# Optimization experiments

Hardware: AMD Instinct MI355X
Metric: run time of the kernel (lower is better)

## Reference

```python
import jax, jax.numpy as jnp
import numpy as np

N = 200000   # nodes
E = 6400000  # edges
F = 128      # input features
H = 16       # hidden dim (fixed in module)
C = 10       # num classes
B = 512      # graphs in batch


def setup_inputs() -> dict:
    key = jax.random.key(0)
    ks = jax.random.split(key, 9)
    x = jax.random.normal(ks[0], (N, F), dtype=jnp.float32)
    edge_index = jax.random.randint(ks[1], (2, E), 0, N, dtype=jnp.int64)
    batch = jnp.sort(jax.random.randint(ks[2], (N,), 0, B, dtype=jnp.int64))
    W1 = jax.random.normal(ks[3], (F, H), dtype=jnp.float32) * 0.1
    b1 = jnp.zeros((H,), dtype=jnp.float32)
    W2 = jax.random.normal(ks[4], (H, H), dtype=jnp.float32) * 0.1
    b2 = jnp.zeros((H,), dtype=jnp.float32)
    Wfc = jax.random.normal(ks[5], (H, C), dtype=jnp.float32) * 0.1
    bfc = jnp.zeros((C,), dtype=jnp.float32)
    return {"x": x, "edge_index": edge_index, "batch": batch,
            "W1": W1, "b1": b1, "W2": W2, "b2": b2, "Wfc": Wfc, "bfc": bfc}


def reference(x, edge_index, batch, W1, b1, W2, b2, Wfc, bfc):
    row, col = edge_index[0], edge_index[1]  # source -> target
    ones_e = jnp.ones((E,), dtype=x.dtype)
    # GCN symmetric norm with implicit self-loops: deg = 1 + in-degree
    deg = 1.0 + jax.ops.segment_sum(ones_e, col, num_segments=N)
    dis = deg ** -0.5                         # [N]
    norm = dis[row] * dis[col]                # [E], self-loop norm = 1/deg

    def gcn_conv(h, W, b):
        hw = h @ W                             # [N, out]
        msg = norm[:, None] * hw[row]          # [E, out]
        agg = jax.ops.segment_sum(msg, col, num_segments=N)
        agg = agg + hw * (1.0 / deg)[:, None]  # self-loop contribution
        return agg + b

    h = jax.nn.relu(gcn_conv(x, W1, b1))
    h = gcn_conv(h, W2, b2)
    # global mean pool over graphs
    ones_n = jnp.ones((N,), dtype=h.dtype)
    counts = jax.ops.segment_sum(ones_n, batch, num_segments=B)
    sums = jax.ops.segment_sum(h, batch, num_segments=B)
    pooled = sums / jnp.maximum(counts, 1.0)[:, None]  # [B, H]
    return pooled @ Wfc + bfc                           # [B, C]
```

## Files before the change

kernel.cpp:

```cpp
#include <hip/hip_runtime.h>

#define N_ 200000
#define E_ 6400000
#define F_ 128
#define H_ 16
#define C_ 10
#define B_ 512

#define CSH   15
#define NCH   7
#define SBSH  11
#define NSB   98
#define NKEY  (NCH * NSB)
#define NT    256
#define EPT   25000
#define N1    (N_ + 1)
#define AGGB  1563
#define G1B   1563
#define QSTR  516

__global__ __launch_bounds__(1024) void k_count1(const int* __restrict__ row, const int* __restrict__ col,
                                                 int* __restrict__ cnt1) {
    __shared__ int hist[NKEY];
    int tid = threadIdx.x, tile = blockIdx.x;
    for (int i = tid; i < NKEY; i += 1024) hist[i] = 0;
    __syncthreads();
    const int* r = row + (size_t)tile * EPT;
    const int* c = col + (size_t)tile * EPT;
    for (int i = tid; i < EPT; i += 1024) {
        int key = (r[i] >> CSH) * NSB + (c[i] >> SBSH);
        atomicAdd(&hist[key], 1);
    }
    __syncthreads();
    for (int i = tid; i < NKEY; i += 1024) cnt1[(size_t)i * NT + tile] = hist[i];
}

__global__ __launch_bounds__(256) void k_scan_col(int* __restrict__ cnt_mat, int* __restrict__ keyTotal) {
    __shared__ int s[256];
    int k = blockIdx.x, t = threadIdx.x;
    int v[4];
    int seg = 0;
#pragma unroll
    for (int j = 0; j < 4; ++j) {
        int idx = 4 * t + j;
        v[j] = (idx < NT) ? cnt_mat[(size_t)k * NT + idx] : 0;
        seg += v[j];
    }
    s[t] = seg;
    __syncthreads();
    for (int off = 1; off < 256; off <<= 1) {
        int tmp = (t >= off) ? s[t - off] : 0;
        __syncthreads();
        s[t] += tmp;
        __syncthreads();
    }
    if (t == 255) keyTotal[k] = s[255];
    int running = s[t] - seg;
#pragma unroll
    for (int j = 0; j < 4; ++j) {
        int idx = 4 * t + j;
        if (idx < NT) {
            int old = v[j];
            cnt_mat[(size_t)k * NT + idx] = running;
            running += old;
        }
    }
}

__global__ __launch_bounds__(1024) void k_scan_top(const int* __restrict__ keyTotal, int* __restrict__ keyStart, int n) {
    __shared__ int s[1024];
    int t = threadIdx.x;
    int v = (t < n) ? keyTotal[t] : 0;
    s[t] = v;
    __syncthreads();
    for (int off = 1; off < 1024; off <<= 1) {
        int tmp = (t >= off) ? s[t - off] : 0;
        __syncthreads();
        s[t] += tmp;
        __syncthreads();
    }
    if (t < n) keyStart[t] = s[t] - v;
    if (t == n - 1) keyStart[n] = s[t];
}

__global__ __launch_bounds__(1024) void k_part1(const int* __restrict__ row, const int* __restrict__ col,
                                                const int* __restrict__ cnt1, const int* __restrict__ ks1,
                                                unsigned int* __restrict__ esrc) {
    __shared__ int cur[NKEY];
    int tid = threadIdx.x, tile = blockIdx.x;
    for (int i = tid; i < NKEY; i += 1024) cur[i] = cnt1[(size_t)i * NT + tile] + ks1[i];
    __syncthreads();
    const int* r = row + (size_t)tile * EPT;
    const int* c = col + (size_t)tile * EPT;
    for (int i = tid; i < EPT; i += 1024) {
        int src = r[i], dst = c[i];
        int key = (src >> CSH) * NSB + (dst >> SBSH);
        int p = atomicAdd(&cur[key], 1);
        esrc[p] = ((unsigned int)(dst & 2047) << CSH) | (unsigned int)(src & 32767);
    }
}

__global__ __launch_bounds__(512) void k_part2(const unsigned int* __restrict__ esrc, const int* __restrict__ ks1,
                                               unsigned short* __restrict__ off16, unsigned int* __restrict__ edges) {
    __shared__ int cnt[2048];
    __shared__ int aux[512];
    int b = blockIdx.x, tid = threadIdx.x;
    int c = b / NSB, sb = b % NSB;
    int s = ks1[b], e = ks1[b + 1], len = e - s;
    if (sb == NSB - 1 && tid == 0) off16[(size_t)c * N1 + N_] = (unsigned short)len;
    for (int i = tid; i < 2048; i += 512) cnt[i] = 0;
    __syncthreads();
    for (int i = tid; i < len; i += 512) atomicAdd(&cnt[esrc[s + i] >> CSH], 1);
    __syncthreads();
    int base = tid * 4;
    int vals[4];
    int run = 0;
#pragma unroll
    for (int j = 0; j < 4; ++j) { vals[j] = cnt[base + j]; run += vals[j]; }
    aux[tid] = run;
    __syncthreads();
    for (int o = 1; o < 512; o <<= 1) {
        int tmp = (tid >= o) ? aux[tid - o] : 0;
        __syncthreads();
        aux[tid] += tmp;
        __syncthreads();
    }
    int acc = aux[tid] - run;
    int nb = (sb << SBSH) + base;
#pragma unroll
    for (int j = 0; j < 4; ++j) {
        int v = vals[j];
        cnt[base + j] = acc;
        int n = nb + j;
        if (n < N_) off16[(size_t)c * N1 + n] = (unsigned short)acc;
        acc += v;
    }
    __syncthreads();
    for (int i = tid; i < len; i += 512) {
        unsigned int w = esrc[s + i];
        int pos = atomicAdd(&cnt[w >> CSH], 1);
        edges[s + pos] = ((unsigned int)c << CSH) | (w & 32767u);
    }
}

__global__ __launch_bounds__(256) void k_gemm1s(const float* __restrict__ x, const float* __restrict__ W1,
                                                const unsigned short* __restrict__ off16, const int* __restrict__ ks1g,
                                                float* __restrict__ dis, float* __restrict__ P) {
    __shared__ float wsh[4 * QSTR];
    __shared__ int ks[NKEY + 1];
    for (int i = threadIdx.x; i < F_ * H_; i += 256) {
        int r = i >> 4, h = i & 15;
        int qq = (r >> 2) & 3, jj = r >> 4, mm = r & 3;
        wsh[qq * QSTR + (jj * 4 + mm) * 16 + h] = W1[i];
    }
    for (int i = threadIdx.x; i <= NKEY; i += 256) ks[i] = ks1g[i];
    __syncthreads();
    int t = blockIdx.x * 256 + threadIdx.x;
    int p = t >> 2, q = t & 3;
    int n0 = p * 2;
    if (n0 >= N_) return;
    int sb00 = n0 >> SBSH, sb01 = (n0 + 1) >> SBSH, sbE = (n0 + 2) >> SBSH;
    int deg0 = 0, deg1 = 0;
    for (int c = q; c < NCH; c += 4) {
        const unsigned short* ob = off16 + (size_t)c * N1 + n0;
        ushort2 o2 = *(const ushort2*)ob;
        unsigned short oE = ob[2];
        deg0 += (ks[c * NSB + sb01] + o2.y) - (ks[c * NSB + sb00] + o2.x);
        deg1 += (ks[c * NSB + sbE] + oE) - (ks[c * NSB + sb01] + o2.y);
    }
    deg0 += __shfl_xor(deg0, 1); deg0 += __shfl_xor(deg0, 2);
    deg1 += __shfl_xor(deg1, 1); deg1 += __shfl_xor(deg1, 2);
    float dn0 = rsqrtf(1.0f + (float)deg0);
    float dn1 = rsqrtf(1.0f + (float)deg1);
    if (q == 0) dis[n0] = dn0;
    if (q == 1) dis[n0 + 1] = dn1;
    const float4* xr0 = (const float4*)(x + (size_t)n0 * F_);
    const float4* xr1 = (const float4*)(x + (size_t)(n0 + 1) * F_);
    const float4* wq = (const float4*)(wsh + q * QSTR);
    float4 a0q0 = {0,0,0,0}, a0q1 = {0,0,0,0}, a0q2 = {0,0,0,0}, a0q3 = {0,0,0,0};
    float4 a1q0 = {0,0,0,0}, a1q1 = {0,0,0,0}, a1q2 = {0,0,0,0}, a1q3 = {0,0,0,0};
#define KSTEP(RL, XS0, XS1)                                                        \
    {                                                                              \
        float4 w0 = wq[(RL) * 4 + 0], w1 = wq[(RL) * 4 + 1];                       \
        float4 w2 = wq[(RL) * 4 + 2], w3 = wq[(RL) * 4 + 3];                       \
        a0q0.x += (XS0) * w0.x; a0q0.y += (XS0) * w0.y; a0q0.z += (XS0) * w0.z; a0q0.w += (XS0) * w0.w; \
        a0q1.x += (XS0) * w1.x; a0q1.y += (XS0) * w1.y; a0q1.z += (XS0) * w1.z; a0q1.w += (XS0) * w1.w; \
        a0q2.x += (XS0) * w2.x; a0q2.y += (XS0) * w2.y; a0q2.z += (XS0) * w2.z; a0q2.w += (XS0) * w2.w; \
        a0q3.x += (XS0) * w3.x; a0q3.y += (XS0) * w3.y; a0q3.z += (XS0) * w3.z; a0q3.w += (XS0) * w3.w; \
        a1q0.x += (XS1) * w0.x; a1q0.y += (XS1) * w0.y; a1q0.z += (XS1) * w0.z; a1q0.w += (XS1) * w0.w; \
        a1q1.x += (XS1) * w1.x; a1q1.y += (XS1) * w1.y; a1q1.z += (XS1) * w1.z; a1q1.w += (XS1) * w1.w; \
        a1q2.x += (XS1) * w2.x; a1q2.y += (XS1) * w2.y; a1q2.z += (XS1) * w2.z; a1q2.w += (XS1) * w2.w; \
        a1q3.x += (XS1) * w3.x; a1q3.y += (XS1) * w3.y; a1q3.z += (XS1) * w3.z; a1q3.w += (XS1) * w3.w; \
    }
#pragma unroll
    for (int j = 0; j < 8; ++j) {
        float4 xa = xr0[j * 4 + q];
        float4 xb = xr1[j * 4 + q];
        int rb = j * 4;
        KSTEP(rb + 0, xa.x, xb.x)
        KSTEP(rb + 1, xa.y, xb.y)
        KSTEP(rb + 2, xa.z, xb.z)
        KSTEP(rb + 3, xa.w, xb.w)
    }
#undef KSTEP
#define RED(F)                                                                     \
    F.x += __shfl_xor(F.x, 1); F.y += __shfl_xor(F.y, 1); F.z += __shfl_xor(F.z, 1); F.w += __shfl_xor(F.w, 1); \
    F.x += __shfl_xor(F.x, 2); F.y += __shfl_xor(F.y, 2); F.z += __shfl_xor(F.z, 2); F.w += __shfl_xor(F.w, 2);
    RED(a0q0) RED(a0q1) RED(a0q2) RED(a0q3)
    RED(a1q0) RED(a1q1) RED(a1q2) RED(a1q3)
#undef RED
    float4 s0 = (q == 0) ? a0q0 : (q == 1) ? a0q1 : (q == 2) ? a0q2 : a0q3;
    float4 s1 = (q == 0) ? a1q0 : (q == 1) ? a1q1 : (q == 2) ? a1q2 : a1q3;
    float4* P4 = (float4*)P;
    float4 o0, o1;
    o0.x = s0.x * dn0; o0.y = s0.y * dn0; o0.z = s0.z * dn0; o0.w = s0.w * dn0;
    o1.x = s1.x * dn1; o1.y = s1.y * dn1; o1.z = s1.z * dn1; o1.w = s1.w * dn1;
    P4[(size_t)n0 * 4 + q] = o0;
    P4[(size_t)(n0 + 1) * 4 + q] = o1;
}

__global__ __launch_bounds__(256) void k_gemm2s(const float* __restrict__ hin, const float* __restrict__ W2,
                                                const float* __restrict__ dis, float* __restrict__ P) {
    __shared__ float w[H_ * H_];
    if (threadIdx.x < H_ * H_) w[threadIdx.x] = W2[threadIdx.x];
    __syncthreads();
    int n = blockIdx.x * 256 + threadIdx.x;
    if (n >= N_) return;
    float hv[H_];
    const float4* hr = reinterpret_cast<const float4*>(hin + (size_t)n * H_);
#pragma unroll
    for (int q = 0; q < 4; ++q) {
        float4 v = hr[q];
        hv[q * 4 + 0] = v.x; hv[q * 4 + 1] = v.y; hv[q * 4 + 2] = v.z; hv[q * 4 + 3] = v.w;
    }
    float acc[H_];
#pragma unroll
    for (int h = 0; h < H_; ++h) acc[h] = 0.f;
#pragma unroll
    for (int k = 0; k < H_; ++k)
#pragma unroll
        for (int h = 0; h < H_; ++h) acc[h] += hv[k] * w[k * H_ + h];
    float dn = dis[n];
    float* o = P + (size_t)n * H_;
#pragma unroll
    for (int h = 0; h < H_; h += 4)
        *(float4*)(o + h) = make_float4(acc[h] * dn, acc[h + 1] * dn, acc[h + 2] * dn, acc[h + 3] * dn);
}

template <int RELU>
__global__ __launch_bounds__(256) void k_agg(const float4* __restrict__ P4, const unsigned int* __restrict__ csr,
                                             const unsigned short* __restrict__ off16, const int* __restrict__ ks1g,
                                             const float* __restrict__ dis, const float* __restrict__ bias,
                                             float4* __restrict__ Q4) {
    __shared__ int ks[NKEY + 1];
    for (int i = threadIdx.x; i <= NKEY; i += 256) ks[i] = ks1g[i];
    __syncthreads();
    int g = threadIdx.x >> 2, hq = threadIdx.x & 3;
    int n0 = blockIdx.x * 128 + g * 2;
    if (n0 >= N_) return;
    int sb  = n0 >> SBSH;
    int sbE = (n0 + 2) >> SBSH;
    float4 acc0 = {0,0,0,0}, acc1 = {0,0,0,0};
    const unsigned short* ob = off16 + n0;
    ushort2 o2 = *(const ushort2*)ob;
    unsigned short oE = ob[2];
#pragma unroll
    for (int c = 0; c < NCH; ++c) {
        int bs = ks[c * NSB + sb];
        int be = ks[c * NSB + sbE];
        int s0 = bs + o2.x;
        int s1 = bs + o2.y;
        int e1 = be + oE;
        if (c + 1 < NCH) {
            const unsigned short* obn = off16 + (size_t)(c + 1) * N1 + n0;
            o2 = *(const ushort2*)obn;
            oE = obn[2];
        }
#pragma unroll 4
        for (int p = s0; p < e1; ++p) {
            float4 v = P4[(size_t)(csr[p] & 0x3FFFFFFFu) * 4 + hq];
            float w0 = (p < s1) ? 1.f : 0.f;
            float w1 = 1.f - w0;
            acc0.x += w0 * v.x; acc0.y += w0 * v.y; acc0.z += w0 * v.z; acc0.w += w0 * v.w;
            acc1.x += w1 * v.x; acc1.y += w1 * v.y; acc1.z += w1 * v.z; acc1.w += w1 * v.w;
        }
    }
    float2 d2 = *(const float2*)(dis + n0);
    float4 b4 = ((const float4*)bias)[hq];
#define FINISH(ACC, K, DN)                                            \
    {                                                                 \
        float4 self = P4[(size_t)(n0 + K) * 4 + hq];                  \
        float4 v;                                                     \
        v.x = (DN) * (ACC.x + self.x) + b4.x;                         \
        v.y = (DN) * (ACC.y + self.y) + b4.y;                         \
        v.z = (DN) * (ACC.z + self.z) + b4.z;                         \
        v.w = (DN) * (ACC.w + self.w) + b4.w;                         \
        if (RELU) {                                                   \
            v.x = fmaxf(v.x, 0.f); v.y = fmaxf(v.y, 0.f);             \
            v.z = fmaxf(v.z, 0.f); v.w = fmaxf(v.w, 0.f);             \
        }                                                             \
        Q4[(size_t)(n0 + K) * 4 + hq] = v;                            \
    }
    FINISH(acc0, 0, d2.x)
    FINISH(acc1, 1, d2.y)
#undef FINISH
}

__global__ __launch_bounds__(256) void k_pool_fc(const float* __restrict__ h2, const int* __restrict__ batch,
                                                 const float* __restrict__ Wfc, const float* __restrict__ bfc,
                                                 float* __restrict__ out) {
    int b = blockIdx.x;
    int lo = 0, hi = N_;
    while (lo < hi) { int m = (lo + hi) >> 1; if (batch[m] < b) lo = m + 1; else hi = m; }
    int start = lo;
    lo = start; hi = N_;
    while (lo < hi) { int m = (lo + hi) >> 1; if (batch[m] < b + 1) lo = m + 1; else hi = m; }
    int end = lo;

    int t = threadIdx.x;
    int h = t & 15, q = t >> 4;
    float acc = 0.f;
    for (int n = start + q; n < end; n += 16) acc += h2[(size_t)n * H_ + h];
    acc += __shfl_xor(acc, 16);
    acc += __shfl_xor(acc, 32);

    __shared__ float part[4][H_];
    __shared__ float pooled[H_];
    if ((t & 63) < 16) part[t >> 6][h] = acc;
    __syncthreads();
    if (t < H_) {
        float s2 = part[0][t] + part[1][t] + part[2][t] + part[3][t];
        pooled[t] = s2 / fmaxf((float)(end - start), 1.0f);
    }
    __syncthreads();
    if (t < C_) {
        float o = bfc[t];
#pragma unroll
        for (int hh = 0; hh < H_; ++hh) o += pooled[hh] * Wfc[hh * C_ + t];
        out[b * C_ + t] = o;
    }
}

extern "C" void kernel_launch(void* const* d_in, const int* in_sizes, int n_in,
                              void* d_out, int out_size, void* d_ws, size_t ws_size,
                              hipStream_t stream) {
    const float* x    = (const float*)d_in[0];
    const int*   ei   = (const int*)d_in[1];
    const int*   batch= (const int*)d_in[2];
    const float* W1   = (const float*)d_in[3];
    const float* b1   = (const float*)d_in[4];
    const float* W2   = (const float*)d_in[5];
    const float* b2   = (const float*)d_in[6];
    const float* Wfc  = (const float*)d_in[7];
    const float* bfc  = (const float*)d_in[8];
    float* out = (float*)d_out;

    const int* row = ei;
    const int* col = ei + E_;

    size_t off = 0;
    auto alloc = [&](size_t bytes) -> void* {
        void* p = (char*)d_ws + off;
        off += (bytes + 255) & ~(size_t)255;
        return p;
    };
    char*           U        = (char*)alloc((size_t)NCH * N1 * 2);
    int*            cnt1     = (int*)U;
    unsigned short* off16    = (unsigned short*)U;
    int*            keyTotal = (int*)alloc((size_t)NKEY * 4);
    int*            ks1      = (int*)alloc((size_t)(NKEY + 1) * 4);
    unsigned int*   edges    = (unsigned int*)alloc((size_t)E_ * 4);
    float*          dis      = (float*)alloc((size_t)N_ * 4);
    float*          P        = (float*)alloc((size_t)N_ * H_ * 4);
    float*          Q        = (float*)alloc((size_t)N_ * H_ * 4);
    unsigned int*   esrc     = (unsigned int*)P;
    (void)ws_size; (void)in_sizes; (void)n_in; (void)out_size;

    const int gridN = (N_ + 255) / 256;

    k_count1  <<<NT, 1024, 0, stream>>>(row, col, cnt1);
    k_scan_col<<<NKEY, 256, 0, stream>>>(cnt1, keyTotal);
    k_scan_top<<<1, 1024, 0, stream>>>(keyTotal, ks1, NKEY);
    k_part1   <<<NT, 1024, 0, stream>>>(row, col, cnt1, ks1, esrc);
    k_part2   <<<NKEY, 512, 0, stream>>>(esrc, ks1, off16, edges);

    k_gemm1s<<<G1B, 256, 0, stream>>>(x, W1, off16, ks1, dis, P);
    k_agg<1><<<AGGB, 256, 0, stream>>>((const float4*)P, edges, off16, ks1, dis, b1, (float4*)Q);
    k_gemm2s<<<gridN, 256, 0, stream>>>(Q, W2, dis, P);
    k_agg<0><<<AGGB, 256, 0, stream>>>((const float4*)P, edges, off16, ks1, dis, b2, (float4*)Q);

    k_pool_fc<<<B_, 256, 0, stream>>>(Q, batch, Wfc, bfc, out);
}
```

Baseline: 290.7 us.

## Halve sub-bucket size and stage second-pass scatter in LDS before coalesced write

Sub-buckets now cover 1024 destination nodes instead of 2048, which doubles the number of keys and second-pass blocks. The top-level scan is rewritten to loop over 1024-wide tiles so it can handle more than 1024 keys. In the second partition pass, buckets that fit in 6144 entries are scattered into shared memory and then written to global memory contiguously, replacing random global writes with coalesced ones. A redundant mask on the CSR index in the aggregation loop is also dropped. The cost is more blocks and more histogram entries in the first pass, plus larger shared-memory use per block.

```diff
diff --git a/kernel.cpp b/kernel.cpp
--- a/kernel.cpp
+++ b/kernel.cpp
@@ -9,12 +9,13 @@
 
 #define CSH   15
 #define NCH   7
-#define SBSH  11
-#define NSB   98
+#define SBSH  10
+#define NSB   196
 #define NKEY  (NCH * NSB)
 #define NT    256
 #define EPT   25000
 #define N1    (N_ + 1)
+#define STG2  6144
 #define AGGB  1563
 #define G1B   1563
 #define QSTR  516
@@ -69,18 +70,28 @@
 
 __global__ __launch_bounds__(1024) void k_scan_top(const int* __restrict__ keyTotal, int* __restrict__ keyStart, int n) {
     __shared__ int s[1024];
+    __shared__ int base;
     int t = threadIdx.x;
-    int v = (t < n) ? keyTotal[t] : 0;
-    s[t] = v;
-    __syncthreads();
-    for (int off = 1; off < 1024; off <<= 1) {
-        int tmp = (t >= off) ? s[t - off] : 0;
-        __syncthreads();
-        s[t] += tmp;
-        __syncthreads();
-    }
-    if (t < n) keyStart[t] = s[t] - v;
-    if (t == n - 1) keyStart[n] = s[t];
+    if (t == 0) base = 0;
+    __syncthreads();
+    int ntile = (n + 1023) / 1024;
+    for (int tile = 0; tile < ntile; ++tile) {
+        int idx = tile * 1024 + t;
+        int v = (idx < n) ? keyTotal[idx] : 0;
+        s[t] = v;
+        __syncthreads();
+        for (int off = 1; off < 1024; off <<= 1) {
+            int tmp = (t >= off) ? s[t - off] : 0;
+            __syncthreads();
+            s[t] += tmp;
+            __syncthreads();
+        }
+        if (idx < n) keyStart[idx] = base + s[t] - v;
+        __syncthreads();
+        if (t == 0) base += s[1023];
+        __syncthreads();
+    }
+    if (t == 0) keyStart[n] = base;
 }
 
 __global__ __launch_bounds__(1024) void k_part1(const int* __restrict__ row, const int* __restrict__ col,
@@ -96,27 +107,27 @@
         int src = r[i], dst = c[i];
         int key = (src >> CSH) * NSB + (dst >> SBSH);
         int p = atomicAdd(&cur[key], 1);
-        esrc[p] = ((unsigned int)(dst & 2047) << CSH) | (unsigned int)(src & 32767);
+        esrc[p] = ((unsigned int)(dst & 1023) << CSH) | (unsigned int)(src & 32767);
     }
 }
 
 __global__ __launch_bounds__(512) void k_part2(const unsigned int* __restrict__ esrc, const int* __restrict__ ks1,
                                                unsigned short* __restrict__ off16, unsigned int* __restrict__ edges) {
-    __shared__ int cnt[2048];
+    __shared__ unsigned int stg[STG2];
+    __shared__ int cnt[1024];
     __shared__ int aux[512];
     int b = blockIdx.x, tid = threadIdx.x;
     int c = b / NSB, sb = b % NSB;
     int s = ks1[b], e = ks1[b + 1], len = e - s;
     if (sb == NSB - 1 && tid == 0) off16[(size_t)c * N1 + N_] = (unsigned short)len;
-    for (int i = tid; i < 2048; i += 512) cnt[i] = 0;
+    cnt[tid] = 0;
+    cnt[tid + 512] = 0;
     __syncthreads();
     for (int i = tid; i < len; i += 512) atomicAdd(&cnt[esrc[s + i] >> CSH], 1);
     __syncthreads();
-    int base = tid * 4;
-    int vals[4];
-    int run = 0;
-#pragma unroll
-    for (int j = 0; j < 4; ++j) { vals[j] = cnt[base + j]; run += vals[j]; }
+    int base = tid * 2;
+    int v0 = cnt[base], v1 = cnt[base + 1];
+    int run = v0 + v1;
     aux[tid] = run;
     __syncthreads();
     for (int o = 1; o < 512; o <<= 1) {
@@ -127,19 +138,26 @@
     }
     int acc = aux[tid] - run;
     int nb = (sb << SBSH) + base;
-#pragma unroll
-    for (int j = 0; j < 4; ++j) {
-        int v = vals[j];
-        cnt[base + j] = acc;
-        int n = nb + j;
-        if (n < N_) off16[(size_t)c * N1 + n] = (unsigned short)acc;
-        acc += v;
-    }
-    __syncthreads();
-    for (int i = tid; i < len; i += 512) {
-        unsigned int w = esrc[s + i];
-        int pos = atomicAdd(&cnt[w >> CSH], 1);
-        edges[s + pos] = ((unsigned int)c << CSH) | (w & 32767u);
+    cnt[base] = acc;
+    if (nb < N_) off16[(size_t)c * N1 + nb] = (unsigned short)acc;
+    acc += v0;
+    cnt[base + 1] = acc;
+    if (nb + 1 < N_) off16[(size_t)c * N1 + nb + 1] = (unsigned short)acc;
+    __syncthreads();
+    if (len <= STG2) {
+        for (int i = tid; i < len; i += 512) {
+            unsigned int w = esrc[s + i];
+            int pos = atomicAdd(&cnt[w >> CSH], 1);
+            stg[pos] = ((unsigned int)c << CSH) | (w & 32767u);
+        }
+        __syncthreads();
+        for (int i = tid; i < len; i += 512) edges[s + i] = stg[i];
+    } else {
+        for (int i = tid; i < len; i += 512) {
+            unsigned int w = esrc[s + i];
+            int pos = atomicAdd(&cnt[w >> CSH], 1);
+            edges[s + pos] = ((unsigned int)c << CSH) | (w & 32767u);
+        }
     }
 }
 
@@ -278,7 +296,7 @@
         }
 #pragma unroll 4
         for (int p = s0; p < e1; ++p) {
-            float4 v = P4[(size_t)(csr[p] & 0x3FFFFFFFu) * 4 + hq];
+            float4 v = P4[(size_t)csr[p] * 4 + hq];
             float w0 = (p < s1) ? 1.f : 0.f;
             float w1 = 1.f - w0;
             acc0.x += w0 * v.x; acc0.y += w0 * v.y; acc0.z += w0 * v.z; acc0.w += w0 * v.w;
```

Result: faster. 268.9 us (-7.5%).
